# Kernel tuning notes

Measured on AMD Instinct MI355X. Metric: run time of the kernel, lower is better.

The kernel has to match this reference:

```python
import jax, jax.numpy as jnp
import numpy as np

B, T = 4, 512
IN, OUT, D, HID = 80, 4096, 512, 1024
E, NB, LPB = 4, 2, 4
NL = NB * LPB
H, M = 8, 64
LB, LA, SL, SR = 4, 1, 2, 1


def setup_inputs():
    key = jax.random.key(0)
    it = iter(jax.random.split(key, 40))
    def nrm(shape, s=0.02):
        return jax.random.normal(next(it), shape, jnp.float32) * s
    return {
        'x': jax.random.normal(next(it), (B, T, IN), jnp.float32),
        'seq_len': jax.random.randint(next(it), (B,), T // 2, T + 1),
        'emb_w1': nrm((IN, HID)), 'emb_b1': jnp.zeros((HID,), jnp.float32),
        'emb_w2': nrm((HID, D)), 'emb_wo': nrm((D, OUT)),
        'f0_w1': nrm((E, IN, HID)), 'f0_b1': jnp.zeros((E, HID), jnp.float32),
        'f0_w2': nrm((E, HID, D)), 'f0_router': nrm((D, E)),
        'f0_fb': nrm((LB, D), 0.1), 'f0_fa': nrm((LA, D), 0.1),
        'f_w1': nrm((NL - 1, E, D, HID)), 'f_b1': jnp.zeros((NL - 1, E, HID), jnp.float32),
        'f_w2': nrm((NL - 1, E, HID, D)), 'f_router': nrm((NL - 1, D, E)),
        'f_fb': nrm((NL - 1, LB, D), 0.1), 'f_fa': nrm((NL - 1, LA, D), 0.1),
        'attn_wq': nrm((NB, D, D)), 'attn_wk': nrm((NB, D, D)),
        'attn_wv': nrm((NB, D, D)), 'attn_wo': nrm((NB, D, D)),
        'attn_mk': nrm((NB, M, D)), 'attn_mv': nrm((NB, M, D)),
        'ln_g': jnp.ones((NB, D), jnp.float32), 'ln_b': jnp.zeros((NB, D), jnp.float32),
        'out_w': nrm((D, OUT)), 'out_b': jnp.zeros((OUT,), jnp.float32),
    }


def _fsmn_memory(p, fb, fa):
    # m[t] = p[t] + sum_k fb[k]*p[t-(k+1)*SL] + sum_j fa[j]*p[t+(j+1)*SR]  (depthwise)
    m = p
    for k in range(fb.shape[0]):
        off = (k + 1) * SL
        past = jnp.pad(p, ((0, 0), (off, 0), (0, 0)))[:, :p.shape[1]]
        m = m + past * fb[k]
    for j in range(fa.shape[0]):
        off = (j + 1) * SR
        fut = jnp.pad(p, ((0, 0), (0, off), (0, 0)))[:, off:]
        m = m + fut * fa[j]
    return m


def _pe(dtype):
    pos = jnp.arange(T, dtype=jnp.float32)[:, None]
    div = jnp.exp(jnp.arange(0, D, 2, dtype=jnp.float32) * (-np.log(10000.0) / D))
    pe = jnp.zeros((T, D), jnp.float32)
    pe = pe.at[:, 0::2].set(jnp.sin(pos * div)).at[:, 1::2].set(jnp.cos(pos * div))
    return pe.astype(dtype)


def _layernorm(x, g, b):
    mu = jnp.mean(x, -1, keepdims=True)
    var = jnp.var(x, -1, keepdims=True)
    return (x - mu) * jax.lax.rsqrt(var + 1e-5) * g + b


def reference(x, seq_len, emb_w1, emb_b1, emb_w2, emb_wo,
              f0_w1, f0_b1, f0_w2, f0_router, f0_fb, f0_fa,
              f_w1, f_b1, f_w2, f_router, f_fb, f_fa,
              attn_wq, attn_wk, attn_wv, attn_wo, attn_mk, attn_mv,
              ln_g, ln_b, out_w, out_b):
    tok_mask = jnp.arange(T)[None, :] < seq_len[:, None]  # [B,T] valid frames

    # embed sub-network (router features; detached as in Net.forward)
    embed = jax.nn.relu(x @ emb_w1 + emb_b1) @ emb_w2      # [B,T,D]
    embed_out = embed @ emb_wo                             # [B,T,OUT]
    embed_r = jax.lax.stop_gradient(embed)

    def moe_fsmn(xi, w1, b1, w2, router, fb, fa, skip):
        gates = jax.nn.softmax(embed_r @ router, axis=-1)  # [B,T,E]
        g = jnp.max(gates, axis=-1)
        disp = jax.nn.one_hot(jnp.argmax(gates, -1), E, dtype=xi.dtype) * g[..., None]
        h = jax.nn.relu(jnp.einsum('bti,eih->beth', xi, w1) + b1[None, :, None, :])
        p = jnp.einsum('beth,ehd->betd', h, w2)            # low-rank expert proj
        p = jnp.einsum('bte,betd->btd', disp, p)           # top-1 combine
        m = _fsmn_memory(p, fb, fa)
        if skip:
            m = m + xi
        imp = jnp.sum(gates * tok_mask[..., None].astype(gates.dtype), axis=(0, 1))
        aux = jnp.var(imp) / (jnp.mean(imp) ** 2 + 1e-9)   # importance cv^2
        return m, aux

    def attention(xi, wq, wk, wv, wo, mk, mv, g, b):
        dh = D // H
        q = (xi @ wq).reshape(B, T, H, dh)
        k = jnp.concatenate([xi @ wk, jnp.broadcast_to(mk, (B, M, D))], 1).reshape(B, T + M, H, dh)
        v = jnp.concatenate([xi @ wv, jnp.broadcast_to(mv, (B, M, D))], 1).reshape(B, T + M, H, dh)
        scores = jnp.einsum('bthd,bshd->bhts', q, k) / np.sqrt(dh).astype(np.float32)
        key_ok = jnp.concatenate([tok_mask, jnp.ones((B, M), bool)], 1)  # memory keys never masked
        scores = jnp.where(key_ok[:, None, None, :], scores, jnp.float32(-1e9))
        a = jax.nn.softmax(scores, -1)
        o = jnp.einsum('bhts,bshd->bthd', a, v).reshape(B, T, D) @ wo
        return _layernorm(xi + o, g, b)

    auxes = []
    cur = x
    li = 0
    for blk in range(NB):
        for _ in range(LPB):
            if li == 0:
                cur, aux = moe_fsmn(cur, f0_w1, f0_b1, f0_w2, f0_router, f0_fb, f0_fa, False)
            else:
                j = li - 1
                cur, aux = moe_fsmn(cur, f_w1[j], f_b1[j], f_w2[j], f_router[j], f_fb[j], f_fa[j], True)
            auxes.append(aux)
            li += 1
        if blk == 0:
            cur = cur + _pe(cur.dtype)[None]
        cur = attention(cur, attn_wq[blk], attn_wk[blk], attn_wv[blk], attn_wo[blk],
                        attn_mk[blk], attn_mv[blk], ln_g[blk], ln_b[blk])
    out = cur @ out_w + out_b
    return out, embed_out, jnp.stack(auxes).sum()
```

## Files before the change

kernel.cpp:

```cpp
#include <hip/hip_runtime.h>
#include <hip/hip_bf16.h>


typedef __bf16 bf16x8 __attribute__((ext_vector_type(8)));
typedef float f32x4 __attribute__((ext_vector_type(4)));

#define B_ 4
#define T_ 512
#define IN_ 80
#define OUT_ 4096
#define D_ 512
#define HID_ 1024
#define E_ 4
#define H_ 8
#define DH_ 64
#define M_ 64
#define BT_ (B_ * T_)
#define TKV_ (T_ + M_)
#define RBLK_ (BT_ / 4)

__device__ __forceinline__ unsigned pk2(float a, float b) {
    unsigned short ua = __builtin_bit_cast(unsigned short, (__bf16)a);
    unsigned short ub = __builtin_bit_cast(unsigned short, (__bf16)b);
    return (unsigned)ua | ((unsigned)ub << 16);
}
__device__ __forceinline__ unsigned pkh2(__bf16 a, __bf16 b) {
    unsigned short ua = __builtin_bit_cast(unsigned short, a);
    unsigned short ub = __builtin_bit_cast(unsigned short, b);
    return (unsigned)ua | ((unsigned)ub << 16);
}

__global__ __launch_bounds__(256) void gemm80_k(
    const float* __restrict__ A,
    const float* __restrict__ Bw,
    const float* __restrict__ bias,
    float* __restrict__ C)
{
    __shared__ float As[80][68];
    __shared__ float Bs[80][68];
    int m0 = blockIdx.y * 64, n0 = blockIdx.x * 64;
    int tid = threadIdx.x;
#pragma unroll
    for (int i = 0; i < 5; i++) {
        int idx = tid + 256 * i;
        int m = idx / 20, c = idx % 20;
        float4 f = *(const float4*)&A[(size_t)(m0 + m) * 80 + c * 4];
        As[c * 4 + 0][m] = f.x; As[c * 4 + 1][m] = f.y;
        As[c * 4 + 2][m] = f.z; As[c * 4 + 3][m] = f.w;
    }
#pragma unroll
    for (int i = 0; i < 5; i++) {
        int idx = tid + 256 * i;
        int k = idx / 16, c = idx % 16;
        float4 f = *(const float4*)&Bw[(size_t)k * 1024 + n0 + c * 4];
        *(float4*)&Bs[k][c * 4] = f;
    }
    __syncthreads();
    int tx = tid & 15, ty = tid >> 4;
    float acc[4][4];
#pragma unroll
    for (int j = 0; j < 4; j++)
#pragma unroll
        for (int i = 0; i < 4; i++) acc[j][i] = 0.f;
#pragma unroll 8
    for (int k = 0; k < 80; k++) {
        float4 a = *(const float4*)&As[k][ty * 4];
        float4 b = *(const float4*)&Bs[k][tx * 4];
        float av[4] = {a.x, a.y, a.z, a.w};
        float bv[4] = {b.x, b.y, b.z, b.w};
#pragma unroll
        for (int j = 0; j < 4; j++)
#pragma unroll
            for (int i = 0; i < 4; i++) acc[j][i] += av[j] * bv[i];
    }
#pragma unroll
    for (int j = 0; j < 4; j++) {
        size_t row = (size_t)(m0 + ty * 4 + j);
        float4 o;
        o.x = fmaxf(acc[j][0] + bias[n0 + tx * 4 + 0], 0.f);
        o.y = fmaxf(acc[j][1] + bias[n0 + tx * 4 + 1], 0.f);
        o.z = fmaxf(acc[j][2] + bias[n0 + tx * 4 + 2], 0.f);
        o.w = fmaxf(acc[j][3] + bias[n0 + tx * 4 + 3], 0.f);
        *(float4*)&C[row * 1024 + n0 + tx * 4] = o;
    }
}

__global__ void wr2_k(const float* __restrict__ w2,
                      const float* __restrict__ r0,
                      const float* __restrict__ rl,
                      float* __restrict__ R2)
{
    int wv = threadIdx.x >> 6, lane = threadIdx.x & 63;
    int h = blockIdx.x * 4 + wv;
    const float* wrow = w2 + (size_t)h * 512;
    float w[8];
#pragma unroll
    for (int i = 0; i < 8; i++) w[i] = wrow[lane + 64 * i];
    for (int l = 0; l < 8; l++) {
        const float* rp = (l == 0) ? r0 : rl + (size_t)(l - 1) * 2048;
        double a0 = 0, a1 = 0, a2 = 0, a3 = 0;
#pragma unroll
        for (int i = 0; i < 8; i++) {
            int d = lane + 64 * i;
            float4 r = *(const float4*)&rp[d * 4];
            a0 += (double)w[i] * (double)r.x;
            a1 += (double)w[i] * (double)r.y;
            a2 += (double)w[i] * (double)r.z;
            a3 += (double)w[i] * (double)r.w;
        }
        for (int off = 32; off; off >>= 1) {
            a0 += __shfl_xor(a0, off); a1 += __shfl_xor(a1, off);
            a2 += __shfl_xor(a2, off); a3 += __shfl_xor(a3, off);
        }
        if (lane == 0) {
            float4 o = make_float4((float)a0, (float)a1, (float)a2, (float)a3);
            *(float4*)&R2[((size_t)l * 1024 + h) * 4] = o;
        }
    }
}

__global__ __launch_bounds__(256) void routerall_k(
    const float* __restrict__ h,
    const float* __restrict__ R2,
    const int* __restrict__ seq_len,
    int* __restrict__ eid,
    float* __restrict__ gatev,
    float* __restrict__ impPart)
{
    __shared__ float impLoc[4][32];
    int wv = threadIdx.x >> 6, lane = threadIdx.x & 63;
    int tok = blockIdx.x * 4 + wv;
    const float* hr = h + (size_t)tok * 1024;
    float acc[8][4];
#pragma unroll
    for (int l = 0; l < 8; l++)
#pragma unroll
        for (int e = 0; e < 4; e++) acc[l][e] = 0.f;
    for (int i = 0; i < 16; i++) {
        int d = lane + 64 * i;
        float hv = hr[d];
#pragma unroll
        for (int l = 0; l < 8; l++) {
            float4 r = *(const float4*)&R2[((size_t)l * 1024 + d) * 4];
            acc[l][0] += hv * r.x; acc[l][1] += hv * r.y;
            acc[l][2] += hv * r.z; acc[l][3] += hv * r.w;
        }
    }
    for (int off = 32; off; off >>= 1) {
#pragma unroll
        for (int l = 0; l < 8; l++)
#pragma unroll
            for (int e = 0; e < 4; e++) acc[l][e] += __shfl_xor(acc[l][e], off);
    }
    if (lane == 0) {
        int b = tok >> 9, t = tok & 511;
        bool valid = t < seq_len[b];
        for (int l = 0; l < 8; l++) {
            float lg[4] = {acc[l][0], acc[l][1], acc[l][2], acc[l][3]};
            float mx = fmaxf(fmaxf(lg[0], lg[1]), fmaxf(lg[2], lg[3]));
            float g[4], s = 0.f;
            for (int e = 0; e < 4; e++) { g[e] = expf(lg[e] - mx); s += g[e]; }
            float inv = 1.f / s;
            int am = 0; float bv = g[0];
            for (int e = 1; e < 4; e++) if (g[e] > bv) { bv = g[e]; am = e; }
            eid[l * BT_ + tok] = am;
            gatev[l * BT_ + tok] = bv * inv;
            for (int e = 0; e < 4; e++)
                impLoc[wv][l * 4 + e] = valid ? g[e] * inv : 0.f;
        }
    }
    __syncthreads();
    int tid = threadIdx.x;
    if (tid < 32) {
        float s = impLoc[0][tid] + impLoc[1][tid] + impLoc[2][tid] + impLoc[3][tid];
        impPart[(size_t)blockIdx.x * 32 + tid] = s;
    }
}

__device__ __forceinline__ void cvt_body(const float* __restrict__ src,
                                         __bf16* __restrict__ dst,
                                         int idx, int nsh, int kpsh, int Ksrc)
{
    int cprsh = nsh - 3;
    int row = idx >> cprsh;
    int chunk = idx & ((1 << cprsh) - 1);
    int e = row >> kpsh, k = row & ((1 << kpsh) - 1);
    int n = chunk * 8;
    uint4 pk;
    if (k < Ksrc) {
        const float* sp = src + (((size_t)e * Ksrc + k) << nsh) + n;
        float4 f0 = *(const float4*)sp;
        float4 f1 = *(const float4*)(sp + 4);
        pk = make_uint4(pk2(f0.x, f0.y), pk2(f0.z, f0.w),
                        pk2(f1.x, f1.y), pk2(f1.z, f1.w));
    } else pk = make_uint4(0, 0, 0, 0);
    *(uint4*)&dst[(((size_t)row) << nsh) + n] = pk;
}

__device__ __forceinline__ void gather_body(const float* __restrict__ src, int lda,
                                            const int* __restrict__ sorted,
                                            __bf16* __restrict__ dst,
                                            int idx, int kpsh, int Ksrc)
{
    int cprsh = kpsh - 3;
    int row = idx >> cprsh;
    int chunk = idx & ((1 << cprsh) - 1);
    int k0 = chunk * 8;
    uint4 pk;
    if (k0 < Ksrc) {
        const float* sp = src + (size_t)sorted[row] * lda + k0;
        float4 f0 = *(const float4*)sp;
        float4 f1 = *(const float4*)(sp + 4);
        pk = make_uint4(pk2(f0.x, f0.y), pk2(f0.z, f0.w),
                        pk2(f1.x, f1.y), pk2(f1.z, f1.w));
    } else pk = make_uint4(0, 0, 0, 0);
    *(uint4*)&dst[((size_t)row << kpsh) + k0] = pk;
}

__global__ void cvtw_k(const float* __restrict__ src, __bf16* __restrict__ dst,
                       int nsh, int kpsh, int Ksrc)
{
    cvt_body(src, dst, blockIdx.x * 256 + threadIdx.x, nsh, kpsh, Ksrc);
}

__global__ void prep_k(const float* __restrict__ w1, const float* __restrict__ w2,
                       const float* __restrict__ Ain, int lda,
                       const int* __restrict__ sorted,
                       __bf16* __restrict__ w1h, __bf16* __restrict__ w2h,
                       __bf16* __restrict__ Ag,
                       int kpsh, int Ks, int nb1, int nb2)
{
    int bx = blockIdx.x;
    if (bx < nb1) {
        cvt_body(w1, w1h, bx * 256 + threadIdx.x, 10, kpsh, Ks);
    } else if (bx < nb1 + nb2) {
        cvt_body(w2, w2h, (bx - nb1) * 256 + threadIdx.x, 9, 10, HID_);
    } else {
        gather_body(Ain, lda, sorted, Ag, (bx - nb1 - nb2) * 256 + threadIdx.x,
                    kpsh, Ks);
    }
}

template<bool W1OUT>
__global__ __launch_bounds__(256) void egemm_k(
    const __bf16* __restrict__ Ag, const __bf16* __restrict__ Bh,
    const float* __restrict__ bias,
    __bf16* __restrict__ Cb, float* __restrict__ Cf,
    int N, int Kpad,
    const int* __restrict__ seg, const int* __restrict__ sorted,
    const float* __restrict__ scale)
{
    __shared__ __align__(16) __bf16 As[2][128 * 64];
    __shared__ __align__(16) __bf16 Bs[2][64 * 64];

    int e = blockIdx.z;
    int row0 = seg[e], cnt = seg[e + 1] - row0;
    int m0 = blockIdx.y * 128;
    if (m0 >= cnt) return;
    int n0 = blockIdx.x * 64;
    const __bf16* Bp = Bh + (size_t)e * Kpad * N;

    int tid = threadIdx.x;
    int arow = tid >> 1, ahalf = tid & 1;
    int mclamp = min(m0 + arow, cnt - 1);
    const __bf16* aptr = Ag + (size_t)(row0 + mclamp) * Kpad + ahalf * 32;
    int asb = arow * 64;
    int ac0 = ahalf * 4;
    int arx = arow & 7;
    int bn = tid & 63, bkc = tid >> 6;
    const __bf16* bptr = Bp + n0 + bn;
    int bsb = bn * 64;
    int brx = bn & 7;

    int lane = tid & 63, wid = tid >> 6;
    int wm = wid & 1, wn = wid >> 1;
    int l15 = lane & 15, quad = lane >> 4;

    int aoff[4][2], boff[2][2];
#pragma unroll
    for (int mt = 0; mt < 4; mt++) {
        int m = wm * 64 + mt * 16 + l15;
#pragma unroll
        for (int s = 0; s < 2; s++)
            aoff[mt][s] = m * 64 + (((s * 4 + quad) ^ (m & 7)) * 8);
    }
#pragma unroll
    for (int nt = 0; nt < 2; nt++) {
        int n = wn * 32 + nt * 16 + l15;
#pragma unroll
        for (int s = 0; s < 2; s++)
            boff[nt][s] = n * 64 + (((s * 4 + quad) ^ (n & 7)) * 8);
    }

    f32x4 acc[4][2];
#pragma unroll
    for (int mt = 0; mt < 4; mt++)
#pragma unroll
        for (int nt = 0; nt < 2; nt++)
#pragma unroll
            for (int r = 0; r < 4; r++) acc[mt][nt][r] = 0.f;

    uint4 rA[4]; unsigned rB[8];
    auto stage = [&](int k0) {
#pragma unroll
        for (int j = 0; j < 4; j++) rA[j] = *(const uint4*)(aptr + k0 + j * 8);
#pragma unroll
        for (int c = 0; c < 2; c++) {
            int kk = k0 + (bkc * 2 + c) * 8;
#pragma unroll
            for (int i = 0; i < 4; i++)
                rB[c * 4 + i] = pkh2(bptr[(size_t)(kk + 2 * i) * N],
                                     bptr[(size_t)(kk + 2 * i + 1) * N]);
        }
    };
    auto commit = [&](int buf) {
#pragma unroll
        for (int j = 0; j < 4; j++)
            *(uint4*)&As[buf][asb + (((ac0 + j) ^ arx) * 8)] = rA[j];
#pragma unroll
        for (int c = 0; c < 2; c++)
            *(uint4*)&Bs[buf][bsb + (((bkc * 2 + c) ^ brx) * 8)] =
                make_uint4(rB[c * 4 + 0], rB[c * 4 + 1], rB[c * 4 + 2], rB[c * 4 + 3]);
    };

    stage(0); commit(0); __syncthreads();
    int nt_ = Kpad >> 6;
    for (int t = 0; t < nt_; t++) {
        int buf = t & 1;
        if (t + 1 < nt_) stage((t + 1) << 6);
        bf16x8 af[4][2], bfr[2][2];
#pragma unroll
        for (int mt = 0; mt < 4; mt++)
#pragma unroll
            for (int s = 0; s < 2; s++)
                af[mt][s] = *(const bf16x8*)&As[buf][aoff[mt][s]];
#pragma unroll
        for (int ntx = 0; ntx < 2; ntx++)
#pragma unroll
            for (int s = 0; s < 2; s++)
                bfr[ntx][s] = *(const bf16x8*)&Bs[buf][boff[ntx][s]];
#pragma unroll
        for (int mt = 0; mt < 4; mt++)
#pragma unroll
            for (int ntx = 0; ntx < 2; ntx++)
#pragma unroll
                for (int s = 0; s < 2; s++)
                    acc[mt][ntx] = __builtin_amdgcn_mfma_f32_16x16x32_bf16(
                        af[mt][s], bfr[ntx][s], acc[mt][ntx], 0, 0, 0);
        if (t + 1 < nt_) commit(buf ^ 1);
        __syncthreads();
    }

#pragma unroll
    for (int mt = 0; mt < 4; mt++) {
#pragma unroll
        for (int r = 0; r < 4; r++) {
            int m = m0 + wm * 64 + mt * 16 + quad * 4 + r;
            if (m >= cnt) continue;
            if (W1OUT) {
                size_t ci = (size_t)(row0 + m);
#pragma unroll
                for (int ntx = 0; ntx < 2; ntx++) {
                    int col = n0 + wn * 32 + ntx * 16 + l15;
                    float v = acc[mt][ntx][r] + bias[e * N + col];
                    Cb[ci * N + col] = (__bf16)fmaxf(v, 0.f);
                }
            } else {
                int tok = sorted[row0 + m];
                float sc = scale[tok];
#pragma unroll
                for (int ntx = 0; ntx < 2; ntx++) {
                    int col = n0 + wn * 32 + ntx * 16 + l15;
                    Cf[(size_t)tok * N + col] = acc[mt][ntx][r] * sc;
                }
            }
        }
    }
}

template<bool BIAS, bool BF16B>
__global__ __launch_bounds__(256) void dgemm_k(
    const float* __restrict__ A,
    const void* __restrict__ Bv,
    const float* __restrict__ bias,
    float* __restrict__ C,
    int N, int K)
{
    __shared__ __align__(16) __bf16 As[2][128 * 64];
    __shared__ __align__(16) __bf16 Bs[2][64 * 64];

    int m0 = blockIdx.y * 128, n0 = blockIdx.x * 64;
    int tid = threadIdx.x;
    int arow = tid >> 1, ahalf = tid & 1;
    const float* aptr = A + (size_t)(m0 + arow) * K + ahalf * 32;
    int asb = arow * 64, ac0 = ahalf * 4, arx = arow & 7;
    int bn = tid & 63, bkc = tid >> 6;
    const __bf16* bh = (const __bf16*)Bv;
    const float*  bf = (const float*)Bv;
    int bsb = bn * 64, brx = bn & 7;

    int lane = tid & 63, wid = tid >> 6;
    int wm = wid & 1, wn = wid >> 1;
    int l15 = lane & 15, quad = lane >> 4;

    int aoff[4][2], boff[2][2];
#pragma unroll
    for (int mt = 0; mt < 4; mt++) {
        int m = wm * 64 + mt * 16 + l15;
#pragma unroll
        for (int s = 0; s < 2; s++)
            aoff[mt][s] = m * 64 + (((s * 4 + quad) ^ (m & 7)) * 8);
    }
#pragma unroll
    for (int nt = 0; nt < 2; nt++) {
        int n = wn * 32 + nt * 16 + l15;
#pragma unroll
        for (int s = 0; s < 2; s++)
            boff[nt][s] = n * 64 + (((s * 4 + quad) ^ (n & 7)) * 8);
    }

    f32x4 acc[4][2];
#pragma unroll
    for (int mt = 0; mt < 4; mt++)
#pragma unroll
        for (int nt = 0; nt < 2; nt++)
#pragma unroll
            for (int r = 0; r < 4; r++) acc[mt][nt][r] = 0.f;

    uint4 rA[4]; unsigned rB[8];
    auto stage = [&](int k0) {
#pragma unroll
        for (int j = 0; j < 4; j++) {
            float4 f0 = *(const float4*)(aptr + k0 + j * 8);
            float4 f1 = *(const float4*)(aptr + k0 + j * 8 + 4);
            rA[j] = make_uint4(pk2(f0.x, f0.y), pk2(f0.z, f0.w),
                               pk2(f1.x, f1.y), pk2(f1.z, f1.w));
        }
#pragma unroll
        for (int c = 0; c < 2; c++) {
            int kk = k0 + (bkc * 2 + c) * 8;
#pragma unroll
            for (int i = 0; i < 4; i++) {
                if (BF16B)
                    rB[c * 4 + i] = pkh2(bh[(size_t)(kk + 2 * i) * N + n0 + bn],
                                         bh[(size_t)(kk + 2 * i + 1) * N + n0 + bn]);
                else
                    rB[c * 4 + i] = pk2(bf[(size_t)(kk + 2 * i) * N + n0 + bn],
                                        bf[(size_t)(kk + 2 * i + 1) * N + n0 + bn]);
            }
        }
    };
    auto commit = [&](int buf) {
#pragma unroll
        for (int j = 0; j < 4; j++)
            *(uint4*)&As[buf][asb + (((ac0 + j) ^ arx) * 8)] = rA[j];
#pragma unroll
        for (int c = 0; c < 2; c++)
            *(uint4*)&Bs[buf][bsb + (((bkc * 2 + c) ^ brx) * 8)] =
                make_uint4(rB[c * 4 + 0], rB[c * 4 + 1], rB[c * 4 + 2], rB[c * 4 + 3]);
    };

    stage(0); commit(0); __syncthreads();
    int nt_ = K >> 6;
    for (int t = 0; t < nt_; t++) {
        int buf = t & 1;
        if (t + 1 < nt_) stage((t + 1) << 6);
        bf16x8 af[4][2], bfr[2][2];
#pragma unroll
        for (int mt = 0; mt < 4; mt++)
#pragma unroll
            for (int s = 0; s < 2; s++)
                af[mt][s] = *(const bf16x8*)&As[buf][aoff[mt][s]];
#pragma unroll
        for (int ntx = 0; ntx < 2; ntx++)
#pragma unroll
            for (int s = 0; s < 2; s++)
                bfr[ntx][s] = *(const bf16x8*)&Bs[buf][boff[ntx][s]];
#pragma unroll
        for (int mt = 0; mt < 4; mt++)
#pragma unroll
            for (int ntx = 0; ntx < 2; ntx++)
#pragma unroll
                for (int s = 0; s < 2; s++)
                    acc[mt][ntx] = __builtin_amdgcn_mfma_f32_16x16x32_bf16(
                        af[mt][s], bfr[ntx][s], acc[mt][ntx], 0, 0, 0);
        if (t + 1 < nt_) commit(buf ^ 1);
        __syncthreads();
    }

#pragma unroll
    for (int mt = 0; mt < 4; mt++) {
#pragma unroll
        for (int r = 0; r < 4; r++) {
            int m = m0 + wm * 64 + mt * 16 + quad * 4 + r;
#pragma unroll
            for (int ntx = 0; ntx < 2; ntx++) {
                int col = n0 + wn * 32 + ntx * 16 + l15;
                float v = acc[mt][ntx][r];
                if (BIAS) v += bias[col];
                C[(size_t)m * N + col] = v;
            }
        }
    }
}

#define MBM 128
#define MBN 64
#define MBK 32
#define LDAS 40

__global__ __launch_bounds__(256) void qkv_k(
    const float* __restrict__ A,
    const float* __restrict__ wq, const float* __restrict__ wk,
    const float* __restrict__ wv,
    float* __restrict__ qo, float* __restrict__ ko, float* __restrict__ vo)
{
    __shared__ __align__(16) __bf16 As[MBM * LDAS];
    __shared__ __align__(16) __bf16 Bs[MBN * LDAS];

    int n0g = blockIdx.x * MBN;
    int which = n0g >> 9;
    int n0 = n0g & 511;
    const float* Bp = (which == 0) ? wq : (which == 1) ? wk : wv;
    float* Cp = (which == 0) ? qo : (which == 1) ? ko : vo;
    int m0 = blockIdx.y * MBM;

    int tid = threadIdx.x;
    int arow = tid >> 1, ahalf = tid & 1;
    const float* aptr = A + (size_t)(m0 + arow) * D_ + ahalf * 16;
    int asw = (arow >> 3) & 3;
    int bn = tid & 63, bkc = tid >> 6;
    int bcs = bkc ^ ((bn >> 3) & 3);

    int lane = tid & 63, wid = tid >> 6;
    int wm = wid & 1, wn = wid >> 1;
    int l15 = lane & 15, quad = lane >> 4;

    int aoff[4], boff[2];
#pragma unroll
    for (int mt = 0; mt < 4; mt++) {
        int m = wm * 64 + mt * 16 + l15;
        aoff[mt] = m * LDAS + (quad ^ ((m >> 3) & 3)) * 8;
    }
#pragma unroll
    for (int nt = 0; nt < 2; nt++) {
        int n = wn * 32 + nt * 16 + l15;
        boff[nt] = n * LDAS + (quad ^ ((n >> 3) & 3)) * 8;
    }

    f32x4 acc[4][2];
#pragma unroll
    for (int mt = 0; mt < 4; mt++)
#pragma unroll
        for (int nt = 0; nt < 2; nt++)
#pragma unroll
            for (int r = 0; r < 4; r++) acc[mt][nt][r] = 0.f;

    for (int k0 = 0; k0 < D_; k0 += MBK) {
#pragma unroll
        for (int cc = 0; cc < 2; cc++) {
            float4 f0 = *(const float4*)(aptr + k0 + cc * 8);
            float4 f1 = *(const float4*)(aptr + k0 + cc * 8 + 4);
            uint4 pk = make_uint4(pk2(f0.x, f0.y), pk2(f0.z, f0.w),
                                  pk2(f1.x, f1.y), pk2(f1.z, f1.w));
            int cs = (ahalf * 2 + cc) ^ asw;
            *(uint4*)&As[arow * LDAS + cs * 8] = pk;
        }
        {
            float f[8];
            int kk = k0 + bkc * 8;
#pragma unroll
            for (int i = 0; i < 8; i++)
                f[i] = Bp[(size_t)(kk + i) * D_ + n0 + bn];
            uint4 pk = make_uint4(pk2(f[0], f[1]), pk2(f[2], f[3]),
                                  pk2(f[4], f[5]), pk2(f[6], f[7]));
            *(uint4*)&Bs[bn * LDAS + bcs * 8] = pk;
        }
        __syncthreads();
        bf16x8 af[4], bfm[2];
#pragma unroll
        for (int mt = 0; mt < 4; mt++) af[mt] = *(const bf16x8*)&As[aoff[mt]];
#pragma unroll
        for (int nt = 0; nt < 2; nt++) bfm[nt] = *(const bf16x8*)&Bs[boff[nt]];
#pragma unroll
        for (int mt = 0; mt < 4; mt++)
#pragma unroll
            for (int nt = 0; nt < 2; nt++)
                acc[mt][nt] = __builtin_amdgcn_mfma_f32_16x16x32_bf16(
                    af[mt], bfm[nt], acc[mt][nt], 0, 0, 0);
        __syncthreads();
    }

#pragma unroll
    for (int mt = 0; mt < 4; mt++) {
#pragma unroll
        for (int r = 0; r < 4; r++) {
            int mi = wm * 64 + mt * 16 + quad * 4 + r;
            int m = m0 + mi;
#pragma unroll
            for (int nt = 0; nt < 2; nt++) {
                int col = n0 + wn * 32 + nt * 16 + l15;
                Cp[(size_t)m * D_ + col] = acc[mt][nt][r];
            }
        }
    }
}

__global__ void bucketall_k(const int* __restrict__ eidA, int* __restrict__ sortedA,
                            int* __restrict__ segA)
{
    __shared__ int cnt[E_]; __shared__ int cur[E_];
    int l = blockIdx.x;
    const int* eid = eidA + l * BT_;
    int* sorted = sortedA + l * BT_;
    int* seg = segA + l * 8;
    int tid = threadIdx.x;
    if (tid < E_) cnt[tid] = 0;
    __syncthreads();
    for (int t = tid; t < BT_; t += 256) atomicAdd(&cnt[eid[t]], 1);
    __syncthreads();
    if (tid == 0) {
        int o = 0;
        for (int e = 0; e < E_; e++) { seg[e] = o; cur[e] = o; o += cnt[e]; }
        seg[E_] = o;
    }
    __syncthreads();
    for (int t = tid; t < BT_; t += 256) {
        int pos = atomicAdd(&cur[eid[t]], 1);
        sorted[pos] = t;
    }
}

__global__ void fsmn_k(const float* __restrict__ p, const float* __restrict__ fb,
                       const float* __restrict__ fa, float* __restrict__ cur,
                       int skip, int pe)
{
    int idx = blockIdx.x * 256 + threadIdx.x;
    int d = idx & 511;
    int t = (idx >> 9) & 511;
    float m = p[idx];
#pragma unroll
    for (int k = 0; k < 4; k++) {
        int tt = t - 2 * (k + 1);
        if (tt >= 0) m += fb[k * D_ + d] * p[idx - D_ * 2 * (k + 1)];
    }
    if (t + 1 < T_) m += fa[d] * p[idx + D_];
    if (skip) m += cur[idx];
    if (pe) {
        float div = expf((float)(d & ~1) * (-9.210340371976184f / (float)D_));
        float ang = (float)t * div;
        m += (d & 1) ? cosf(ang) : sinf(ang);
    }
    cur[idx] = m;
}

#define QR 16
__global__ __launch_bounds__(256) void attn_k(
    const float* __restrict__ q, const float* __restrict__ kbuf,
    const float* __restrict__ vbuf, const float* __restrict__ mk,
    const float* __restrict__ mv, const int* __restrict__ seq_len,
    float* __restrict__ attno)
{
    __shared__ float kv[64 * 68];
    __shared__ float qs[QR][68];
    __shared__ float sc[QR][584];
    int b = blockIdx.z, h = blockIdx.y, t0 = blockIdx.x * QR;
    int tid = threadIdx.x, w = tid >> 6, lane = tid & 63;
    int r0 = w * 4;
#pragma unroll
    for (int i = 0; i < 4; i++) {
        int idx = tid + 256 * i;
        int r = idx >> 6, d = idx & 63;
        qs[r][d] = q[((size_t)(b * T_) + t0 + r) * D_ + h * DH_ + d] * 0.125f;
    }
    int sl = seq_len[b];
    int ntv = (sl + 63) >> 6;
    int kg = lane & 15, quad = lane >> 4;
    int myrow = r0 + quad;

    for (int ti = 0; ti <= ntv; ti++) {
        int t = (ti < ntv) ? ti : 8;
        int s0 = t * 64;
        __syncthreads();
        {
            const float* kp = (t < 8)
                ? kbuf + ((size_t)(b * T_) + s0 + w * 16) * D_ + h * DH_ + lane
                : mk + (size_t)(w * 16) * D_ + h * DH_ + lane;
#pragma unroll
            for (int jj = 0; jj < 4; jj++) {
                float4 kf;
                kf.x = kp[(jj * 4 + 0) * D_];
                kf.y = kp[(jj * 4 + 1) * D_];
                kf.z = kp[(jj * 4 + 2) * D_];
                kf.w = kp[(jj * 4 + 3) * D_];
                *(float4*)&kv[lane * 68 + w * 16 + jj * 4] = kf;
            }
        }
        __syncthreads();
        float a0 = 0, a1 = 0, a2 = 0, a3 = 0;
#pragma unroll 8
        for (int d = 0; d < 64; d++) {
            float4 kf = *(const float4*)&kv[d * 68 + kg * 4];
            float qv = qs[myrow][d];
            a0 = fmaf(qv, kf.x, a0);
            a1 = fmaf(qv, kf.y, a1);
            a2 = fmaf(qv, kf.z, a2);
            a3 = fmaf(qv, kf.w, a3);
        }
        int sb = s0 + kg * 4;
        float4 o;
        o.x = (sb + 0 >= T_ || sb + 0 < sl) ? a0 : -1e9f;
        o.y = (sb + 1 >= T_ || sb + 1 < sl) ? a1 : -1e9f;
        o.z = (sb + 2 >= T_ || sb + 2 < sl) ? a2 : -1e9f;
        o.w = (sb + 3 >= T_ || sb + 3 < sl) ? a3 : -1e9f;
        *(float4*)&sc[myrow][s0 + kg * 4] = o;
    }
    __syncthreads();

    float inv[4];
#pragma unroll
    for (int r = 0; r < 4; r++) {
        float mx = -1e30f;
        for (int ti = 0; ti <= ntv; ti++) {
            int s0 = ((ti < ntv) ? ti : 8) * 64;
            mx = fmaxf(mx, sc[r0 + r][s0 + lane]);
        }
        for (int off = 32; off; off >>= 1) mx = fmaxf(mx, __shfl_xor(mx, off));
        float sum = 0.f;
        for (int ti = 0; ti <= ntv; ti++) {
            int s0 = ((ti < ntv) ? ti : 8) * 64;
            float e2 = expf(sc[r0 + r][s0 + lane] - mx);
            sc[r0 + r][s0 + lane] = e2; sum += e2;
        }
        for (int off = 32; off; off >>= 1) sum += __shfl_xor(sum, off);
        inv[r] = 1.f / sum;
    }

    float o0 = 0, o1 = 0, o2 = 0, o3 = 0;
    for (int ti = 0; ti <= ntv; ti++) {
        int t = (ti < ntv) ? ti : 8;
        int s0 = t * 64;
        __syncthreads();
#pragma unroll
        for (int i = 0; i < 16; i++) {
            int idx = tid + 256 * i;
            int key = idx >> 6, d = idx & 63;
            const float* vp = (t < 8)
                ? vbuf + ((size_t)(b * T_) + s0 + key) * D_ + h * DH_ + d
                : mv + (size_t)key * D_ + h * DH_ + d;
            kv[key * 68 + d] = *vp;
        }
        __syncthreads();
#pragma unroll 4
        for (int g = 0; g < 16; g++) {
            float4 p0 = *(const float4*)&sc[r0 + 0][s0 + g * 4];
            float4 p1 = *(const float4*)&sc[r0 + 1][s0 + g * 4];
            float4 p2 = *(const float4*)&sc[r0 + 2][s0 + g * 4];
            float4 p3 = *(const float4*)&sc[r0 + 3][s0 + g * 4];
            float v0 = kv[(g * 4 + 0) * 68 + lane];
            float v1 = kv[(g * 4 + 1) * 68 + lane];
            float v2 = kv[(g * 4 + 2) * 68 + lane];
            float v3 = kv[(g * 4 + 3) * 68 + lane];
            o0 += p0.x * v0 + p0.y * v1 + p0.z * v2 + p0.w * v3;
            o1 += p1.x * v0 + p1.y * v1 + p1.z * v2 + p1.w * v3;
            o2 += p2.x * v0 + p2.y * v1 + p2.z * v2 + p2.w * v3;
            o3 += p3.x * v0 + p3.y * v1 + p3.z * v2 + p3.w * v3;
        }
    }
    size_t base = ((size_t)(b * T_) + t0 + r0) * D_ + h * DH_ + lane;
    attno[base + 0 * D_] = o0 * inv[0];
    attno[base + 1 * D_] = o1 * inv[1];
    attno[base + 2 * D_] = o2 * inv[2];
    attno[base + 3 * D_] = o3 * inv[3];
}

__global__ void ln_k(const float* __restrict__ o, const float* __restrict__ g,
                     const float* __restrict__ bb, float* __restrict__ cur)
{
    int w = threadIdx.x >> 6, lane = threadIdx.x & 63;
    size_t row = (size_t)(blockIdx.x * 4 + w);
    float v[8]; float s = 0.f;
#pragma unroll
    for (int i = 0; i < 8; i++) {
        int d = lane + 64 * i;
        v[i] = cur[row * D_ + d] + o[row * D_ + d];
        s += v[i];
    }
    for (int off = 32; off; off >>= 1) s += __shfl_xor(s, off);
    float mu = s * (1.f / D_);
    float vs = 0.f;
#pragma unroll
    for (int i = 0; i < 8; i++) { float dd = v[i] - mu; vs += dd * dd; }
    for (int off = 32; off; off >>= 1) vs += __shfl_xor(vs, off);
    float rstd = rsqrtf(vs * (1.f / D_) + 1e-5f);
#pragma unroll
    for (int i = 0; i < 8; i++) {
        int d = lane + 64 * i;
        cur[row * D_ + d] = (v[i] - mu) * rstd * g[d] + bb[d];
    }
}

__global__ __launch_bounds__(256) void aux_k(const float* __restrict__ impPart,
                                             float* __restrict__ outp)
{
    __shared__ float red[8][32];
    __shared__ float imp[32];
    int tid = threadIdx.x;
    int c = tid & 31, p = tid >> 5;
    float s = 0.f;
    for (int b = p; b < RBLK_; b += 8) s += impPart[(size_t)b * 32 + c];
    red[p][c] = s;
    __syncthreads();
    if (tid < 32) {
        float t = 0.f;
#pragma unroll
        for (int i = 0; i < 8; i++) t += red[i][tid];
        imp[tid] = t;
    }
    __syncthreads();
    if (tid == 0) {
        float total = 0.f;
        for (int l = 0; l < 8; l++) {
            const float* ip = imp + l * 4;
            float m = (ip[0] + ip[1] + ip[2] + ip[3]) * 0.25f;
            float var = 0.f;
            for (int e = 0; e < 4; e++) { float d = ip[e] - m; var += d * d; }
            var *= 0.25f;
            total += var / (m * m + 1e-9f);
        }
        *outp = total;
    }
}

extern "C" void kernel_launch(void* const* d_in, const int* in_sizes, int n_in,
                              void* d_out, int out_size, void* d_ws, size_t ws_size,
                              hipStream_t stream)
{
    (void)in_sizes; (void)n_in; (void)out_size; (void)ws_size;
    const float* x        = (const float*)d_in[0];
    const int*   seqlen   = (const int*)d_in[1];
    const float* emb_w1   = (const float*)d_in[2];
    const float* emb_b1   = (const float*)d_in[3];
    const float* emb_w2   = (const float*)d_in[4];
    const float* emb_wo   = (const float*)d_in[5];
    const float* f0_w1    = (const float*)d_in[6];
    const float* f0_b1    = (const float*)d_in[7];
    const float* f0_w2    = (const float*)d_in[8];
    const float* f0_router= (const float*)d_in[9];
    const float* f0_fb    = (const float*)d_in[10];
    const float* f0_fa    = (const float*)d_in[11];
    const float* f_w1     = (const float*)d_in[12];
    const float* f_b1     = (const float*)d_in[13];
    const float* f_w2     = (const float*)d_in[14];
    const float* f_router = (const float*)d_in[15];
    const float* f_fb     = (const float*)d_in[16];
    const float* f_fa     = (const float*)d_in[17];
    const float* attn_wq  = (const float*)d_in[18];
    const float* attn_wk  = (const float*)d_in[19];
    const float* attn_wv  = (const float*)d_in[20];
    const float* attn_wo  = (const float*)d_in[21];
    const float* attn_mk  = (const float*)d_in[22];
    const float* attn_mv  = (const float*)d_in[23];
    const float* ln_g     = (const float*)d_in[24];
    const float* ln_b     = (const float*)d_in[25];
    const float* out_w    = (const float*)d_in[26];
    const float* out_b    = (const float*)d_in[27];

    float* out0 = (float*)d_out;
    float* out1 = out0 + (size_t)BT_ * OUT_;
    float* out2 = out1 + (size_t)BT_ * OUT_;

    float* fws = (float*)d_ws;
    size_t o = 0;
    float* embedF = fws + o; o += (size_t)BT_ * D_;
    float* curB   = fws + o; o += (size_t)BT_ * D_;
    float* hbuf   = fws + o; o += (size_t)BT_ * HID_;
    float* pbuf   = fws + o; o += (size_t)BT_ * D_;
    float* kbuf   = fws + o; o += (size_t)BT_ * D_;
    float* vbuf   = fws + o; o += (size_t)BT_ * D_;
    float* gatev  = fws + o; o += (size_t)8 * BT_;
    float* impPart= fws + o; o += (size_t)RBLK_ * 32;
    float* R2     = fws + o; o += (size_t)8 * 1024 * 4;
    int* eid     = (int*)(fws + o); o += (size_t)8 * BT_;
    int* sortedA = (int*)(fws + o); o += (size_t)8 * BT_;
    int* segA    = (int*)(fws + o); o += 64;
    __bf16* Ag    = (__bf16*)hbuf;
    __bf16* hbufh = (__bf16*)(hbuf + (size_t)BT_ * D_ / 2);
    __bf16* w1h   = (__bf16*)kbuf;
    __bf16* w2h   = (__bf16*)vbuf;
    __bf16* w2e_h = (__bf16*)vbuf;
    __bf16* woe_h = (__bf16*)kbuf;
    __bf16* outw_h= (__bf16*)kbuf;
    float* qbuf  = pbuf;
    float* attno = hbuf;
    float* tmpo  = hbuf + (size_t)BT_ * D_;

    gemm80_k<<<dim3(HID_ / 64, BT_ / 64, 1), 256, 0, stream>>>(x, emb_w1, emb_b1, hbuf);
    wr2_k<<<256, 256, 0, stream>>>(emb_w2, f0_router, f_router, R2);
    routerall_k<<<RBLK_, 256, 0, stream>>>(hbuf, R2, seqlen, eid, gatev, impPart);
    bucketall_k<<<8, 256, 0, stream>>>(eid, sortedA, segA);
    cvtw_k<<<256, 256, 0, stream>>>(emb_w2, w2e_h, 9, 10, HID_);
    cvtw_k<<<1024, 256, 0, stream>>>(emb_wo, woe_h, 12, 9, D_);
    dgemm_k<false,true><<<dim3(D_ / 64, BT_ / 128, 1), 256, 0, stream>>>(
        hbuf, w2e_h, nullptr, embedF, D_, HID_);
    dgemm_k<false,true><<<dim3(OUT_ / 64, BT_ / 128, 1), 256, 0, stream>>>(
        embedF, woe_h, nullptr, out1, OUT_, D_);

    for (int l = 0; l < 8; l++) {
        const float* w1  = (l == 0) ? f0_w1 : f_w1 + (size_t)(l-1) * E_ * D_ * HID_;
        const float* b1p = (l == 0) ? f0_b1 : f_b1 + (size_t)(l-1) * E_ * HID_;
        const float* w2  = (l == 0) ? f0_w2 : f_w2 + (size_t)(l-1) * E_ * HID_ * D_;
        const float* fbp = (l == 0) ? f0_fb : f_fb + (size_t)(l-1) * 4 * D_;
        const float* fap = (l == 0) ? f0_fa : f_fa + (size_t)(l-1) * 1 * D_;
        const float* Ain = (l == 0) ? x : curB;
        int lda  = (l == 0) ? IN_ : D_;
        int Ks   = (l == 0) ? IN_ : D_;
        int Kp   = (l == 0) ? 128 : 512;
        int kpsh = (l == 0) ? 7 : 9;
        const int* seg = segA + l * 8;
        const int* sorted = sortedA + l * BT_;

        int nb1 = E_ * Kp * HID_ / 8 / 256;
        int nb2 = E_ * HID_ * D_ / 8 / 256;
        int nb3 = BT_ * Kp / 8 / 256;
        prep_k<<<nb1 + nb2 + nb3, 256, 0, stream>>>(
            w1, w2, Ain, lda, sorted, w1h, w2h, Ag, kpsh, Ks, nb1, nb2);

        egemm_k<true><<<dim3(HID_/64, BT_/128, E_), 256, 0, stream>>>(
            Ag, w1h, b1p, hbufh, nullptr, HID_, Kp, seg, nullptr, nullptr);
        egemm_k<false><<<dim3(D_/64, BT_/128, E_), 256, 0, stream>>>(
            hbufh, w2h, nullptr, nullptr, pbuf, D_, HID_, seg, sorted,
            gatev + l * BT_);
        fsmn_k<<<BT_*D_/256, 256, 0, stream>>>(pbuf, fbp, fap, curB,
                                               (l > 0) ? 1 : 0, (l == 3) ? 1 : 0);

        if (l == 3 || l == 7) {
            int ab = (l == 3) ? 0 : 1;
            const float* wq = attn_wq + (size_t)ab * D_ * D_;
            const float* wk = attn_wk + (size_t)ab * D_ * D_;
            const float* wv = attn_wv + (size_t)ab * D_ * D_;
            const float* wo = attn_wo + (size_t)ab * D_ * D_;
            const float* mk = attn_mk + (size_t)ab * M_ * D_;
            const float* mv = attn_mv + (size_t)ab * M_ * D_;
            const float* g  = ln_g + (size_t)ab * D_;
            const float* bb = ln_b + (size_t)ab * D_;

            qkv_k<<<dim3(3 * D_ / MBN, BT_ / MBM, 1), 256, 0, stream>>>(
                curB, wq, wk, wv, qbuf, kbuf, vbuf);
            attn_k<<<dim3(T_/QR, H_, B_), 256, 0, stream>>>(
                qbuf, kbuf, vbuf, mk, mv, seqlen, attno);
            dgemm_k<false,false><<<dim3(D_ / 64, BT_ / 128, 1), 256, 0, stream>>>(
                attno, wo, nullptr, tmpo, D_, D_);
            ln_k<<<BT_/4, 256, 0, stream>>>(tmpo, g, bb, curB);
        }
    }

    cvtw_k<<<1024, 256, 0, stream>>>(out_w, outw_h, 12, 9, D_);
    dgemm_k<true,true><<<dim3(OUT_ / 64, BT_ / 128, 1), 256, 0, stream>>>(
        curB, outw_h, out_b, out0, OUT_, D_);
    aux_k<<<1, 256, 0, stream>>>(impPart, out2);
}
```

Baseline: 1.384 ms.

## Halve expert GEMM M-tile and use online softmax in attention

The expert GEMM M tile is cut from 128 to 64 rows, which launches twice as many blocks over the ragged per-expert segments and wastes fewer padded rows. The cost is less A/B reuse per block and more redundant loads of B. Attention switches from storing the full score matrix in shared memory to a streaming online-softmax with running max and sum. This shrinks shared memory from about 37KB to about 22KB, which may raise occupancy, and removes the separate softmax passes, at the cost of per-tile exp rescaling and extra shuffles.

```diff
diff --git a/kernel.cpp b/kernel.cpp
--- a/kernel.cpp
+++ b/kernel.cpp
@@ -250,22 +250,22 @@
     const int* __restrict__ seg, const int* __restrict__ sorted,
     const float* __restrict__ scale)
 {
-    __shared__ __align__(16) __bf16 As[2][128 * 64];
+    __shared__ __align__(16) __bf16 As[2][64 * 64];
     __shared__ __align__(16) __bf16 Bs[2][64 * 64];
 
     int e = blockIdx.z;
     int row0 = seg[e], cnt = seg[e + 1] - row0;
-    int m0 = blockIdx.y * 128;
+    int m0 = blockIdx.y * 64;
     if (m0 >= cnt) return;
     int n0 = blockIdx.x * 64;
     const __bf16* Bp = Bh + (size_t)e * Kpad * N;
 
     int tid = threadIdx.x;
-    int arow = tid >> 1, ahalf = tid & 1;
+    int arow = tid >> 2, aq = tid & 3;
     int mclamp = min(m0 + arow, cnt - 1);
-    const __bf16* aptr = Ag + (size_t)(row0 + mclamp) * Kpad + ahalf * 32;
+    const __bf16* aptr = Ag + (size_t)(row0 + mclamp) * Kpad + aq * 16;
     int asb = arow * 64;
-    int ac0 = ahalf * 4;
+    int ac0 = aq * 2;
     int arx = arow & 7;
     int bn = tid & 63, bkc = tid >> 6;
     const __bf16* bptr = Bp + n0 + bn;
@@ -276,10 +276,10 @@
     int wm = wid & 1, wn = wid >> 1;
     int l15 = lane & 15, quad = lane >> 4;
 
-    int aoff[4][2], boff[2][2];
-#pragma unroll
-    for (int mt = 0; mt < 4; mt++) {
-        int m = wm * 64 + mt * 16 + l15;
+    int aoff[2][2], boff[2][2];
+#pragma unroll
+    for (int mt = 0; mt < 2; mt++) {
+        int m = wm * 32 + mt * 16 + l15;
 #pragma unroll
         for (int s = 0; s < 2; s++)
             aoff[mt][s] = m * 64 + (((s * 4 + quad) ^ (m & 7)) * 8);
@@ -292,18 +292,18 @@
             boff[nt][s] = n * 64 + (((s * 4 + quad) ^ (n & 7)) * 8);
     }
 
-    f32x4 acc[4][2];
-#pragma unroll
-    for (int mt = 0; mt < 4; mt++)
+    f32x4 acc[2][2];
+#pragma unroll
+    for (int mt = 0; mt < 2; mt++)
 #pragma unroll
         for (int nt = 0; nt < 2; nt++)
 #pragma unroll
             for (int r = 0; r < 4; r++) acc[mt][nt][r] = 0.f;
 
-    uint4 rA[4]; unsigned rB[8];
+    uint4 rA[2]; unsigned rB[8];
     auto stage = [&](int k0) {
 #pragma unroll
-        for (int j = 0; j < 4; j++) rA[j] = *(const uint4*)(aptr + k0 + j * 8);
+        for (int j = 0; j < 2; j++) rA[j] = *(const uint4*)(aptr + k0 + j * 8);
 #pragma unroll
         for (int c = 0; c < 2; c++) {
             int kk = k0 + (bkc * 2 + c) * 8;
@@ -315,7 +315,7 @@
     };
     auto commit = [&](int buf) {
 #pragma unroll
-        for (int j = 0; j < 4; j++)
+        for (int j = 0; j < 2; j++)
             *(uint4*)&As[buf][asb + (((ac0 + j) ^ arx) * 8)] = rA[j];
 #pragma unroll
         for (int c = 0; c < 2; c++)
@@ -328,9 +328,9 @@
     for (int t = 0; t < nt_; t++) {
         int buf = t & 1;
         if (t + 1 < nt_) stage((t + 1) << 6);
-        bf16x8 af[4][2], bfr[2][2];
-#pragma unroll
-        for (int mt = 0; mt < 4; mt++)
+        bf16x8 af[2][2], bfr[2][2];
+#pragma unroll
+        for (int mt = 0; mt < 2; mt++)
 #pragma unroll
             for (int s = 0; s < 2; s++)
                 af[mt][s] = *(const bf16x8*)&As[buf][aoff[mt][s]];
@@ -340,7 +340,7 @@
             for (int s = 0; s < 2; s++)
                 bfr[ntx][s] = *(const bf16x8*)&Bs[buf][boff[ntx][s]];
 #pragma unroll
-        for (int mt = 0; mt < 4; mt++)
+        for (int mt = 0; mt < 2; mt++)
 #pragma unroll
             for (int ntx = 0; ntx < 2; ntx++)
 #pragma unroll
@@ -352,10 +352,10 @@
     }
 
 #pragma unroll
-    for (int mt = 0; mt < 4; mt++) {
+    for (int mt = 0; mt < 2; mt++) {
 #pragma unroll
         for (int r = 0; r < 4; r++) {
-            int m = m0 + wm * 64 + mt * 16 + quad * 4 + r;
+            int m = m0 + wm * 32 + mt * 16 + quad * 4 + r;
             if (m >= cnt) continue;
             if (W1OUT) {
                 size_t ci = (size_t)(row0 + m);
@@ -663,7 +663,7 @@
 {
     __shared__ float kv[64 * 68];
     __shared__ float qs[QR][68];
-    __shared__ float sc[QR][584];
+    __shared__ float pt[4][4][68];
     int b = blockIdx.z, h = blockIdx.y, t0 = blockIdx.x * QR;
     int tid = threadIdx.x, w = tid >> 6, lane = tid & 63;
     int r0 = w * 4;
@@ -677,6 +677,9 @@
     int ntv = (sl + 63) >> 6;
     int kg = lane & 15, quad = lane >> 4;
     int myrow = r0 + quad;
+
+    float Mrow = -1e30f, Srow = 0.f;
+    float o0 = 0, o1 = 0, o2 = 0, o3 = 0;
 
     for (int ti = 0; ti <= ntv; ti++) {
         int t = (ti < ntv) ? ti : 8;
@@ -708,70 +711,65 @@
             a3 = fmaf(qv, kf.w, a3);
         }
         int sb = s0 + kg * 4;
-        float4 o;
-        o.x = (sb + 0 >= T_ || sb + 0 < sl) ? a0 : -1e9f;
-        o.y = (sb + 1 >= T_ || sb + 1 < sl) ? a1 : -1e9f;
-        o.z = (sb + 2 >= T_ || sb + 2 < sl) ? a2 : -1e9f;
-        o.w = (sb + 3 >= T_ || sb + 3 < sl) ? a3 : -1e9f;
-        *(float4*)&sc[myrow][s0 + kg * 4] = o;
-    }
-    __syncthreads();
-
-    float inv[4];
-#pragma unroll
-    for (int r = 0; r < 4; r++) {
-        float mx = -1e30f;
-        for (int ti = 0; ti <= ntv; ti++) {
-            int s0 = ((ti < ntv) ? ti : 8) * 64;
-            mx = fmaxf(mx, sc[r0 + r][s0 + lane]);
-        }
-        for (int off = 32; off; off >>= 1) mx = fmaxf(mx, __shfl_xor(mx, off));
-        float sum = 0.f;
-        for (int ti = 0; ti <= ntv; ti++) {
-            int s0 = ((ti < ntv) ? ti : 8) * 64;
-            float e2 = expf(sc[r0 + r][s0 + lane] - mx);
-            sc[r0 + r][s0 + lane] = e2; sum += e2;
-        }
-        for (int off = 32; off; off >>= 1) sum += __shfl_xor(sum, off);
-        inv[r] = 1.f / sum;
-    }
-
-    float o0 = 0, o1 = 0, o2 = 0, o3 = 0;
-    for (int ti = 0; ti <= ntv; ti++) {
-        int t = (ti < ntv) ? ti : 8;
-        int s0 = t * 64;
+        if (!(sb + 0 >= T_ || sb + 0 < sl)) a0 = -1e9f;
+        if (!(sb + 1 >= T_ || sb + 1 < sl)) a1 = -1e9f;
+        if (!(sb + 2 >= T_ || sb + 2 < sl)) a2 = -1e9f;
+        if (!(sb + 3 >= T_ || sb + 3 < sl)) a3 = -1e9f;
+        float tmax = fmaxf(fmaxf(a0, a1), fmaxf(a2, a3));
+#pragma unroll
+        for (int off = 1; off < 16; off <<= 1)
+            tmax = fmaxf(tmax, __shfl_xor(tmax, off));
+        float Mnew = fmaxf(Mrow, tmax);
+        float p0 = expf(a0 - Mnew), p1 = expf(a1 - Mnew);
+        float p2 = expf(a2 - Mnew), p3 = expf(a3 - Mnew);
+        float f = expf(Mrow - Mnew);
+        float ts = p0 + p1 + p2 + p3;
+#pragma unroll
+        for (int off = 1; off < 16; off <<= 1) ts += __shfl_xor(ts, off);
+        Srow = Srow * f + ts;
+        Mrow = Mnew;
+        *(float4*)&pt[w][quad][kg * 4] = make_float4(p0, p1, p2, p3);
+        float fr0 = __shfl(f, 0),  fr1 = __shfl(f, 16);
+        float fr2 = __shfl(f, 32), fr3 = __shfl(f, 48);
         __syncthreads();
-#pragma unroll
-        for (int i = 0; i < 16; i++) {
-            int idx = tid + 256 * i;
-            int key = idx >> 6, d = idx & 63;
-            const float* vp = (t < 8)
-                ? vbuf + ((size_t)(b * T_) + s0 + key) * D_ + h * DH_ + d
-                : mv + (size_t)key * D_ + h * DH_ + d;
-            kv[key * 68 + d] = *vp;
+        {
+#pragma unroll
+            for (int i = 0; i < 16; i++) {
+                int idx = tid + 256 * i;
+                int key = idx >> 6, d = idx & 63;
+                const float* vp = (t < 8)
+                    ? vbuf + ((size_t)(b * T_) + s0 + key) * D_ + h * DH_ + d
+                    : mv + (size_t)key * D_ + h * DH_ + d;
+                kv[key * 68 + d] = *vp;
+            }
         }
         __syncthreads();
+        o0 *= fr0; o1 *= fr1; o2 *= fr2; o3 *= fr3;
 #pragma unroll 4
         for (int g = 0; g < 16; g++) {
-            float4 p0 = *(const float4*)&sc[r0 + 0][s0 + g * 4];
-            float4 p1 = *(const float4*)&sc[r0 + 1][s0 + g * 4];
-            float4 p2 = *(const float4*)&sc[r0 + 2][s0 + g * 4];
-            float4 p3 = *(const float4*)&sc[r0 + 3][s0 + g * 4];
+            float4 p0v = *(const float4*)&pt[w][0][g * 4];
+            float4 p1v = *(const float4*)&pt[w][1][g * 4];
+            float4 p2v = *(const float4*)&pt[w][2][g * 4];
+            float4 p3v = *(const float4*)&pt[w][3][g * 4];
             float v0 = kv[(g * 4 + 0) * 68 + lane];
             float v1 = kv[(g * 4 + 1) * 68 + lane];
             float v2 = kv[(g * 4 + 2) * 68 + lane];
             float v3 = kv[(g * 4 + 3) * 68 + lane];
-            o0 += p0.x * v0 + p0.y * v1 + p0.z * v2 + p0.w * v3;
-            o1 += p1.x * v0 + p1.y * v1 + p1.z * v2 + p1.w * v3;
-            o2 += p2.x * v0 + p2.y * v1 + p2.z * v2 + p2.w * v3;
-            o3 += p3.x * v0 + p3.y * v1 + p3.z * v2 + p3.w * v3;
-        }
-    }
+            o0 += p0v.x * v0 + p0v.y * v1 + p0v.z * v2 + p0v.w * v3;
+            o1 += p1v.x * v0 + p1v.y * v1 + p1v.z * v2 + p1v.w * v3;
+            o2 += p2v.x * v0 + p2v.y * v1 + p2v.z * v2 + p2v.w * v3;
+            o3 += p3v.x * v0 + p3v.y * v1 + p3v.z * v2 + p3v.w * v3;
+        }
+    }
+    float i0 = 1.f / __shfl(Srow, 0);
+    float i1 = 1.f / __shfl(Srow, 16);
+    float i2 = 1.f / __shfl(Srow, 32);
+    float i3 = 1.f / __shfl(Srow, 48);
     size_t base = ((size_t)(b * T_) + t0 + r0) * D_ + h * DH_ + lane;
-    attno[base + 0 * D_] = o0 * inv[0];
-    attno[base + 1 * D_] = o1 * inv[1];
-    attno[base + 2 * D_] = o2 * inv[2];
-    attno[base + 3 * D_] = o3 * inv[3];
+    attno[base + 0 * D_] = o0 * i0;
+    attno[base + 1 * D_] = o1 * i1;
+    attno[base + 2 * D_] = o2 * i2;
+    attno[base + 3 * D_] = o3 * i3;
 }
 
 __global__ void ln_k(const float* __restrict__ o, const float* __restrict__ g,
@@ -926,9 +924,9 @@
         prep_k<<<nb1 + nb2 + nb3, 256, 0, stream>>>(
             w1, w2, Ain, lda, sorted, w1h, w2h, Ag, kpsh, Ks, nb1, nb2);
 
-        egemm_k<true><<<dim3(HID_/64, BT_/128, E_), 256, 0, stream>>>(
+        egemm_k<true><<<dim3(HID_/64, BT_/64, E_), 256, 0, stream>>>(
             Ag, w1h, b1p, hbufh, nullptr, HID_, Kp, seg, nullptr, nullptr);
-        egemm_k<false><<<dim3(D_/64, BT_/128, E_), 256, 0, stream>>>(
+        egemm_k<false><<<dim3(D_/64, BT_/64, E_), 256, 0, stream>>>(
             hbufh, w2h, nullptr, nullptr, pbuf, D_, HID_, seg, sorted,
             gatev + l * BT_);
         fsmn_k<<<BT_*D_/256, 256, 0, stream>>>(pbuf, fbp, fap, curB,
```

Measured after the change: 1.309 ms. 5.4% less time.
